# Performance work log

Hardware: AMD Instinct MI355X
Metric: run time of the kernel (lower is better)

The kernel has to match this reference:

```python
import jax, jax.numpy as jnp
import numpy as np

H, D, DM, L, B = 16, 64, 1024, 256, 64
SCALE = 1.0 / np.sqrt(D)   # 1/sqrt(d_head)
CHUNK = 64
LN_EPS = 1e-5


def setup_inputs() -> dict:
    key = jax.random.key(0)
    k0, k1, k2, k3 = jax.random.split(key, 4)
    h = jax.random.normal(k0, (L, B, DM), jnp.float32)
    qkv_w = jax.random.normal(k1, (H * 4 * D, DM), jnp.float32) * 0.02
    o_w = jax.random.normal(k2, (DM, H * D), jnp.float32) * 0.02
    ln_gamma = jnp.ones((DM,), jnp.float32)
    ln_beta = jnp.zeros((DM,), jnp.float32)
    pi0 = jax.random.uniform(k3, (H, 256), jnp.float32)
    return {"h": h, "qkv_w": qkv_w, "o_w": o_w,
            "ln_gamma": ln_gamma, "ln_beta": ln_beta, "pi0": pi0}


def _phi(x):
    # elu(x) + 1, then sum-normalize over feature dim
    e = jax.nn.elu(x) + 1.0
    return e / e.sum(-1, keepdims=True)


def _fast_weight_sum(q, k, v):
    # q,k,v: [B,H,L,D]. out[t] = q_t @ W_t, W_t = sum_{s<=t} k_s v_s^T (inclusive).
    # Chunked-recurrent form: intra-chunk causal GEMM + inter-chunk carried state.
    Bb, Hh, Ll, Dd = q.shape
    nc = Ll // CHUNK
    rs = lambda x: x.reshape(Bb, Hh, nc, CHUNK, Dd).transpose(2, 0, 1, 3, 4)  # [nc,B,H,C,D]
    qc, kc, vc = rs(q), rs(k), rs(v)
    mask = jnp.tril(jnp.ones((CHUNK, CHUNK), q.dtype))  # inclusive causal

    def step(W, xs):
        qi, ki, vi = xs  # [B,H,C,D]
        scores = jnp.einsum('bhtd,bhsd->bhts', qi, ki) * mask
        out = jnp.einsum('bhts,bhsd->bhtd', scores, vi) \
            + jnp.einsum('bhtd,bhde->bhte', qi, W)
        W = W + jnp.einsum('bhsd,bhse->bhde', ki, vi)
        return W, out

    W0 = jnp.zeros((Bb, Hh, Dd, Dd), q.dtype)
    _, outs = jax.lax.scan(step, W0, (qc, kc, vc))  # outs: [nc,B,H,C,D]
    return outs.transpose(1, 2, 0, 3, 4).reshape(Bb, Hh, Ll, Dd)


def reference(h, qkv_w, o_w, ln_gamma, ln_beta, pi0):
    slen, bsz, _ = h.shape
    # qkv projection and head split (rbf2keys: q, k1, k2, v)
    qkv = (h @ qkv_w.T).reshape(slen, bsz, H, 4 * D)
    hq, hk1, hk2, hv = jnp.split(qkv, 4, axis=-1)       # each [L,B,H,D]
    perm = lambda x: x.transpose(1, 2, 0, 3)            # -> [B,H,L,D]
    hq, hk1, hk2, hv = perm(hq), perm(hk1), perm(hk2), perm(hv)

    hq = _phi(hq)
    hk1 = _phi(hk1)
    hk2 = _phi(hk2)

    out1 = _fast_weight_sum(hq, hk1, hv)
    out2 = _fast_weight_sum(hq, hk2, hv)

    # skip_attn_normalization=True path: pi0-gated mixture of the two memories
    p = jnp.clip(pi0, 0.0, 1.0)[None, :, :slen, None]   # [1,H,L,1]
    layer_out = SCALE * (out1 * p + out2 * (1.0 - p))   # [B,H,L,D]

    # [B,H,L,D] -> [L,B,H*D]
    layer_out = layer_out.transpose(0, 2, 1, 3).reshape(bsz, slen, H * D).transpose(1, 0, 2)
    attn_out = layer_out @ o_w.T                        # [L,B,DM]

    # post-LN residual (pre_lnorm=False)
    x = h + attn_out
    mu = x.mean(-1, keepdims=True)
    var = ((x - mu) ** 2).mean(-1, keepdims=True)
    return (x - mu) / jnp.sqrt(var + LN_EPS) * ln_gamma + ln_beta
```

## Files before the change

kernel.cpp:

```cpp
#include <hip/hip_runtime.h>
#include <type_traits>


typedef short v8s __attribute__((ext_vector_type(8)));
typedef float v4f __attribute__((ext_vector_type(4)));

__device__ __forceinline__ float bf2f(short s) {
    unsigned int u = ((unsigned int)(unsigned short)s) << 16;
    float f;
    __builtin_memcpy(&f, &u, 4);
    return f;
}
__device__ __forceinline__ short f2bf(float f) {
    unsigned int u;
    __builtin_memcpy(&u, &f, 4);
    u = u + 0x7fffu + ((u >> 16) & 1u);
    return (short)(u >> 16);
}

__device__ __forceinline__ void load_lds16(const short* g, short* l) {
    __builtin_amdgcn_global_load_lds((const __attribute__((address_space(1))) void*)g,
                                     (__attribute__((address_space(3))) void*)l, 16, 0, 0);
}

__global__ void __launch_bounds__(256)
cvt_bf16(const float* __restrict__ in, short* __restrict__ out, int n4) {
    int i = blockIdx.x * 256 + threadIdx.x;
    if (i >= n4) return;
    float4 v = ((const float4*)in)[i];
    short4 o;
    o.x = f2bf(v.x); o.y = f2bf(v.y); o.z = f2bf(v.z); o.w = f2bf(v.w);
    ((short4*)out)[i] = o;
}

template <typename OutT>
__global__ void __launch_bounds__(256)
gemm_nt(const short* __restrict__ A, const short* __restrict__ B,
        OutT* __restrict__ C, int M, int N, int K) {
    constexpr int BM = 128, BK = 32;
    __shared__ __align__(16) short sA[BM * BK];
    __shared__ __align__(16) short sB[BM * BK];
    const int tid = threadIdx.x;
    const int bm = blockIdx.x, bn = blockIdx.y;
    const int lane = tid & 63, w = tid >> 6;
    const int wy = w >> 1, wx = w & 1;
    const int lr = lane & 15, lq = lane >> 4;

    v4f acc[4][4] = {};

    const int srow = 32 * w + (lane >> 2);
    const int scol = (lane & 3) * 8;
    const short* gA0 = A + (long)(bm * BM + srow) * K + scol;
    const short* gB0 = B + (long)(bn * BM + srow) * K + scol;
    short* lA0 = sA + 32 * w * BK;
    short* lB0 = sB + 32 * w * BK;

    for (int kt = 0; kt < K; kt += BK) {
        __syncthreads();
        load_lds16(gA0 + kt, lA0);
        load_lds16(gA0 + 16 * K + kt, lA0 + 16 * BK);
        load_lds16(gB0 + kt, lB0);
        load_lds16(gB0 + 16 * K + kt, lB0 + 16 * BK);
        __syncthreads();

        v8s af[4], bfv[4];
#pragma unroll
        for (int i = 0; i < 4; i++)
            af[i] = *(const v8s*)&sA[(wy * 64 + i * 16 + lr) * BK + lq * 8];
#pragma unroll
        for (int j = 0; j < 4; j++)
            bfv[j] = *(const v8s*)&sB[(wx * 64 + j * 16 + lr) * BK + lq * 8];
#pragma unroll
        for (int i = 0; i < 4; i++)
#pragma unroll
            for (int j = 0; j < 4; j++)
                acc[i][j] = __builtin_amdgcn_mfma_f32_16x16x32_bf16(af[i], bfv[j], acc[i][j], 0, 0, 0);
    }
#pragma unroll
    for (int i = 0; i < 4; i++)
#pragma unroll
        for (int j = 0; j < 4; j++)
#pragma unroll
            for (int r = 0; r < 4; r++) {
                int row = bm * BM + wy * 64 + i * 16 + lq * 4 + r;
                int col = bn * BM + wx * 64 + j * 16 + lr;
                float v = acc[i][j][r];
                if constexpr (std::is_same_v<OutT, short>)
                    C[(long)row * N + col] = f2bf(v);
                else
                    C[(long)row * N + col] = v;
            }
}

#define SW(row, s) ((row) * 72 + ((((s) >> 3) ^ (((row) >> 4) & 7)) << 3) + ((s) & 7))

__global__ void __launch_bounds__(256)
fastweight(const short* __restrict__ qkv, short* __restrict__ out1, short* __restrict__ out2) {
    const int bid = blockIdx.x;
    const int mem = bid & 1, h = (bid >> 1) & 15, b = bid >> 5;
    const int tid = threadIdx.x;
    const int w = tid >> 6, lane = tid & 63;
    const int lq = lane >> 4, lr = lane & 15;
    __shared__ __align__(16) short sq[64 * 72];
    __shared__ __align__(16) short skS[64 * 72];
    __shared__ __align__(16) short skT[64 * 72];
    __shared__ __align__(16) short svT[64 * 72];
    __shared__ __align__(16) short sWT[64 * 72];
    short* outbuf = mem ? out2 : out1;
    const int koff = 64 + mem * 64;

    for (int i = tid; i < 64 * 36; i += 256) ((int*)sWT)[i] = 0;

    const int r = tid >> 2, seg = (tid & 3) * 16;

    v4f wacc[4] = {};

    for (int c = 0; c < 4; c++) {
        __syncthreads();
        const long gbase = ((long)((c * 64 + r) * 64 + b)) * 4096 + h * 256;
        {
            union { int4 v[2]; short s[16]; } u;
            u.v[0] = *(const int4*)(qkv + gbase + seg);
            u.v[1] = *(const int4*)(qkv + gbase + seg + 8);
            float f[16]; float ssum = 0.f;
#pragma unroll
            for (int i = 0; i < 16; i++) {
                float x = bf2f(u.s[i]);
                float e = x > 0.f ? x + 1.f : __expf(x);
                f[i] = e; ssum += e;
            }
            ssum += __shfl_xor(ssum, 1, 64);
            ssum += __shfl_xor(ssum, 2, 64);
            float inv = 1.f / ssum;
            union { int4 v[2]; short s[16]; } o;
#pragma unroll
            for (int i = 0; i < 16; i++) o.s[i] = f2bf(f[i] * inv);
            *(int4*)&sq[SW(r, seg)] = o.v[0];
            *(int4*)&sq[SW(r, seg + 8)] = o.v[1];
        }
        {
            union { int4 v[2]; short s[16]; } u;
            u.v[0] = *(const int4*)(qkv + gbase + koff + seg);
            u.v[1] = *(const int4*)(qkv + gbase + koff + seg + 8);
            float f[16]; float ssum = 0.f;
#pragma unroll
            for (int i = 0; i < 16; i++) {
                float x = bf2f(u.s[i]);
                float e = x > 0.f ? x + 1.f : __expf(x);
                f[i] = e; ssum += e;
            }
            ssum += __shfl_xor(ssum, 1, 64);
            ssum += __shfl_xor(ssum, 2, 64);
            float inv = 1.f / ssum;
            union { int4 v[2]; short s[16]; } o;
#pragma unroll
            for (int i = 0; i < 16; i++) o.s[i] = f2bf(f[i] * inv);
            *(int4*)&skS[SW(r, seg)] = o.v[0];
            *(int4*)&skS[SW(r, seg + 8)] = o.v[1];
#pragma unroll
            for (int i = 0; i < 16; i++) skT[SW(seg + i, r)] = o.s[i];
        }
        {
            union { int4 v[2]; short s[16]; } u;
            u.v[0] = *(const int4*)(qkv + gbase + 192 + seg);
            u.v[1] = *(const int4*)(qkv + gbase + 192 + seg + 8);
#pragma unroll
            for (int i = 0; i < 16; i++) svT[SW(seg + i, r)] = u.s[i];
        }
        __syncthreads();

        v8s qa0 = *(const v8s*)&sq[SW(16 * w + lr, lq * 8)];
        v8s qa1 = *(const v8s*)&sq[SW(16 * w + lr, 32 + lq * 8)];

        v4f sacc[4];
#pragma unroll
        for (int n = 0; n < 4; n++) {
            v8s b0 = *(const v8s*)&skS[SW(16 * n + lr, lq * 8)];
            v8s b1 = *(const v8s*)&skS[SW(16 * n + lr, 32 + lq * 8)];
            v4f t = {};
            t = __builtin_amdgcn_mfma_f32_16x16x32_bf16(qa0, b0, t, 0, 0, 0);
            t = __builtin_amdgcn_mfma_f32_16x16x32_bf16(qa1, b1, t, 0, 0, 0);
            sacc[n] = t;
        }
        __syncthreads();
#pragma unroll
        for (int n = 0; n < 4; n++)
#pragma unroll
            for (int rr = 0; rr < 4; rr++) {
                int t_ = 16 * w + lq * 4 + rr;
                int s_ = 16 * n + lr;
                skS[SW(t_, s_)] = f2bf(s_ <= t_ ? sacc[n][rr] : 0.f);
            }

        v8s sa0 = *(const v8s*)&skS[SW(16 * w + lr, lq * 8)];
        v8s sa1 = *(const v8s*)&skS[SW(16 * w + lr, 32 + lq * 8)];
        v4f oacc[4];
#pragma unroll
        for (int n = 0; n < 4; n++) {
            v8s vb0 = *(const v8s*)&svT[SW(16 * n + lr, lq * 8)];
            v8s vb1 = *(const v8s*)&svT[SW(16 * n + lr, 32 + lq * 8)];
            v8s wb0 = *(const v8s*)&sWT[SW(16 * n + lr, lq * 8)];
            v8s wb1 = *(const v8s*)&sWT[SW(16 * n + lr, 32 + lq * 8)];
            v4f t = {};
            t = __builtin_amdgcn_mfma_f32_16x16x32_bf16(sa0, vb0, t, 0, 0, 0);
            t = __builtin_amdgcn_mfma_f32_16x16x32_bf16(sa1, vb1, t, 0, 0, 0);
            t = __builtin_amdgcn_mfma_f32_16x16x32_bf16(qa0, wb0, t, 0, 0, 0);
            t = __builtin_amdgcn_mfma_f32_16x16x32_bf16(qa1, wb1, t, 0, 0, 0);
            oacc[n] = t;
        }
#pragma unroll
        for (int n = 0; n < 4; n++)
#pragma unroll
            for (int rr = 0; rr < 4; rr++) {
                int t_ = 16 * w + lq * 4 + rr;
                long o = ((long)((c * 64 + t_) * 64 + b)) * 1024 + h * 64 + 16 * n + lr;
                outbuf[o] = f2bf(oacc[n][rr]);
            }

        if (c < 3) {
            __syncthreads();
            v8s va0 = *(const v8s*)&svT[SW(16 * w + lr, lq * 8)];
            v8s va1 = *(const v8s*)&svT[SW(16 * w + lr, 32 + lq * 8)];
#pragma unroll
            for (int n = 0; n < 4; n++) {
                v8s kb0 = *(const v8s*)&skT[SW(16 * n + lr, lq * 8)];
                v8s kb1 = *(const v8s*)&skT[SW(16 * n + lr, 32 + lq * 8)];
                wacc[n] = __builtin_amdgcn_mfma_f32_16x16x32_bf16(va0, kb0, wacc[n], 0, 0, 0);
                wacc[n] = __builtin_amdgcn_mfma_f32_16x16x32_bf16(va1, kb1, wacc[n], 0, 0, 0);
            }
#pragma unroll
            for (int n = 0; n < 4; n++)
#pragma unroll
                for (int rr = 0; rr < 4; rr++)
                    sWT[SW(16 * w + lq * 4 + rr, 16 * n + lr)] = f2bf(wacc[n][rr]);
        }
    }
}

__global__ void __launch_bounds__(256)
mix_kernel(const short* __restrict__ l1, const short* __restrict__ l2,
           const float* __restrict__ pi0, short* __restrict__ outm) {
    long idx8 = ((long)blockIdx.x * 256 + threadIdx.x) * 8;
    int col = (int)(idx8 & 1023);
    int row = (int)(idx8 >> 10);
    int hh = col >> 6;
    int l = row >> 6;
    float p = pi0[hh * 256 + l];
    p = fminf(fmaxf(p, 0.f), 1.f);
    float q = 1.f - p;
    union { int4 v; short s[8]; } ua, ub, uo;
    ua.v = *(const int4*)(l1 + idx8);
    ub.v = *(const int4*)(l2 + idx8);
#pragma unroll
    for (int i = 0; i < 8; i++)
        uo.s[i] = f2bf(0.125f * (p * bf2f(ua.s[i]) + q * bf2f(ub.s[i])));
    *(int4*)(outm + idx8) = uo.v;
}

__global__ void __launch_bounds__(256)
ln_kernel(const float* __restrict__ h, const float* __restrict__ attn,
          const float* __restrict__ gamma, const float* __restrict__ beta,
          float* __restrict__ out) {
    const int row = blockIdx.x;
    const long base = (long)row * 1024;
    const int tid = threadIdx.x;
    float4 xh = ((const float4*)(h + base))[tid];
    float4 xa = ((const float4*)(attn + base))[tid];
    float4 x;
    x.x = xh.x + xa.x; x.y = xh.y + xa.y; x.z = xh.z + xa.z; x.w = xh.w + xa.w;
    float s = x.x + x.y + x.z + x.w;
    float s2 = x.x * x.x + x.y * x.y + x.z * x.z + x.w * x.w;
#pragma unroll
    for (int m = 32; m > 0; m >>= 1) {
        s += __shfl_xor(s, m, 64);
        s2 += __shfl_xor(s2, m, 64);
    }
    __shared__ float ps[4], ps2[4];
    int w = tid >> 6, lane = tid & 63;
    if (lane == 0) { ps[w] = s; ps2[w] = s2; }
    __syncthreads();
    s = ps[0] + ps[1] + ps[2] + ps[3];
    s2 = ps2[0] + ps2[1] + ps2[2] + ps2[3];
    float mu = s * (1.f / 1024.f);
    float var = s2 * (1.f / 1024.f) - mu * mu;
    float inv = rsqrtf(var + 1e-5f);
    float4 g = ((const float4*)gamma)[tid];
    float4 bb = ((const float4*)beta)[tid];
    float4 o;
    o.x = (x.x - mu) * inv * g.x + bb.x;
    o.y = (x.y - mu) * inv * g.y + bb.y;
    o.z = (x.z - mu) * inv * g.z + bb.z;
    o.w = (x.w - mu) * inv * g.w + bb.w;
    ((float4*)(out + base))[tid] = o;
}

extern "C" void kernel_launch(void* const* d_in, const int* in_sizes, int n_in,
                              void* d_out, int out_size, void* d_ws, size_t ws_size,
                              hipStream_t stream) {
    const float* h     = (const float*)d_in[0];
    const float* qkvw  = (const float*)d_in[1];
    const float* ow    = (const float*)d_in[2];
    const float* gamma = (const float*)d_in[3];
    const float* beta  = (const float*)d_in[4];
    const float* pi0   = (const float*)d_in[5];
    float* out = (float*)d_out;
    char* ws = (char*)d_ws;

    short* h_bf   = (short*)(ws);
    short* wq_bf  = (short*)(ws + 33554432);
    short* wo_bf  = (short*)(ws + 41943040);
    short* qkv_bf = (short*)(ws + 44040192);
    short* l1     = (short*)(ws + 178257920);
    short* l2     = (short*)(ws + 211812352);
    float* attnf  = (float*)(ws + 44040192);
    short* lmix   = h_bf;

    cvt_bf16<<<16384, 256, 0, stream>>>(h, h_bf, 16777216 / 4);
    cvt_bf16<<<4096, 256, 0, stream>>>(qkvw, wq_bf, 4194304 / 4);
    cvt_bf16<<<1024, 256, 0, stream>>>(ow, wo_bf, 1048576 / 4);

    gemm_nt<short><<<dim3(128, 32), 256, 0, stream>>>(h_bf, wq_bf, qkv_bf, 16384, 4096, 1024);

    fastweight<<<2048, 256, 0, stream>>>(qkv_bf, l1, l2);

    mix_kernel<<<8192, 256, 0, stream>>>(l1, l2, pi0, lmix);

    gemm_nt<float><<<dim3(128, 8), 256, 0, stream>>>(lmix, wo_bf, attnf, 16384, 1024, 1024);

    ln_kernel<<<16384, 256, 0, stream>>>(h, attnf, gamma, beta, out);
}
```

Baseline: 463.1 us.

## Rewrite bf16 GEMM as 256x256 double-buffered pipelined kernel with swizzled LDS

Replaces the simple 128x128 tile GEMM, which synchronises twice per K step, with a 256x256 tile, 512-thread kernel. It double-buffers LDS with a 64-wide K tile, interleaves global-to-LDS staging with MFMA quarters under explicit barriers and vmcnt waits, XOR-swizzles LDS to avoid bank conflicts, and remaps block IDs for L2 locality. The aim is to hide load latency and raise MFMA utilisation in both projection GEMMs. The cost is heavy register pressure from 32 accumulator tiles and 128 KB of LDS, which permits only one block per CU, plus fragile hand-tuned synchronisation.

```diff
diff --git a/kernel.cpp b/kernel.cpp
--- a/kernel.cpp
+++ b/kernel.cpp
@@ -34,57 +34,126 @@
 }
 
 template <typename OutT>
-__global__ void __launch_bounds__(256)
-gemm_nt(const short* __restrict__ A, const short* __restrict__ B,
+__global__ void __launch_bounds__(512, 2)
+gemm_nt(const short* __restrict__ Ap, const short* __restrict__ Bp,
         OutT* __restrict__ C, int M, int N, int K) {
-    constexpr int BM = 128, BK = 32;
-    __shared__ __align__(16) short sA[BM * BK];
-    __shared__ __align__(16) short sB[BM * BK];
+    __shared__ __align__(16) short lds[2][2][256 * 64];
+
     const int tid = threadIdx.x;
-    const int bm = blockIdx.x, bn = blockIdx.y;
-    const int lane = tid & 63, w = tid >> 6;
-    const int wy = w >> 1, wx = w & 1;
-    const int lr = lane & 15, lq = lane >> 4;
-
-    v4f acc[4][4] = {};
-
-    const int srow = 32 * w + (lane >> 2);
-    const int scol = (lane & 3) * 8;
-    const short* gA0 = A + (long)(bm * BM + srow) * K + scol;
-    const short* gB0 = B + (long)(bn * BM + srow) * K + scol;
-    short* lA0 = sA + 32 * w * BK;
-    short* lB0 = sB + 32 * w * BK;
-
-    for (int kt = 0; kt < K; kt += BK) {
-        __syncthreads();
-        load_lds16(gA0 + kt, lA0);
-        load_lds16(gA0 + 16 * K + kt, lA0 + 16 * BK);
-        load_lds16(gB0 + kt, lB0);
-        load_lds16(gB0 + 16 * K + kt, lB0 + 16 * BK);
-        __syncthreads();
-
-        v8s af[4], bfv[4];
-#pragma unroll
-        for (int i = 0; i < 4; i++)
-            af[i] = *(const v8s*)&sA[(wy * 64 + i * 16 + lr) * BK + lq * 8];
-#pragma unroll
-        for (int j = 0; j < 4; j++)
-            bfv[j] = *(const v8s*)&sB[(wx * 64 + j * 16 + lr) * BK + lq * 8];
-#pragma unroll
-        for (int i = 0; i < 4; i++)
-#pragma unroll
-            for (int j = 0; j < 4; j++)
-                acc[i][j] = __builtin_amdgcn_mfma_f32_16x16x32_bf16(af[i], bfv[j], acc[i][j], 0, 0, 0);
+    const int w = tid >> 6, lane = tid & 63;
+    const int wm = w >> 2, wn = w & 3;
+    const int lq = lane >> 4, lr = lane & 15;
+    const int asw = (lr & 7) * 8;
+    const int rr = tid >> 3;
+    const int scol = ((tid & 7) * 8) ^ ((rr & 7) * 8);
+
+    int bid = blockIdx.y * gridDim.x + blockIdx.x;
+    int nwg = gridDim.x * gridDim.y;
+    int swz = (bid & 7) * (nwg >> 3) + (bid >> 3);
+    int bm = swz % gridDim.x, bn = swz / gridDim.x;
+
+    v4f acc[8][4] = {};
+    v8s a[4][2];
+    v8s b[2][2][2];
+
+    const int NT = K >> 6;
+    const int nIter = NT >> 1;
+
+#define BAR_() do { asm volatile("" ::: "memory"); __builtin_amdgcn_s_barrier(); asm volatile("" ::: "memory"); } while (0)
+#define VMCNT4_() asm volatile("s_waitcnt vmcnt(4)" ::: "memory")
+#define STAGE_(MAT, BUF, HALF, KT) do { \
+        const short* g_ = ((MAT) ? Bp : Ap) + \
+            (long)(((MAT) ? bn : bm) * 256 + (HALF) * 128 + rr) * K + (KT) * 64 + scol; \
+        short* l_ = &lds[BUF][MAT][(HALF) * 8192] + w * 512; \
+        load_lds16(g_, l_); \
+        load_lds16(g_ + (long)64 * K, l_ + 4096); \
+    } while (0)
+#define LDA_(QM, BUF) do { \
+        _Pragma("unroll") \
+        for (int mi = 0; mi < 4; ++mi) { \
+            const short* pa_ = &lds[BUF][0][(wm * 128 + (QM) * 64 + mi * 16 + lr) * 64]; \
+            a[mi][0] = *(const v8s*)&pa_[(lq * 8) ^ asw]; \
+            a[mi][1] = *(const v8s*)&pa_[(32 + lq * 8) ^ asw]; \
+        } \
+    } while (0)
+#define LDB_(QN, BUF) do { \
+        _Pragma("unroll") \
+        for (int ni = 0; ni < 2; ++ni) { \
+            const short* pb_ = &lds[BUF][1][(wn * 64 + (QN) * 32 + ni * 16 + lr) * 64]; \
+            b[QN][ni][0] = *(const v8s*)&pb_[(lq * 8) ^ asw]; \
+            b[QN][ni][1] = *(const v8s*)&pb_[(32 + lq * 8) ^ asw]; \
+        } \
+    } while (0)
+#define MFMA_(QM, QN) do { \
+        __builtin_amdgcn_s_setprio(1); \
+        _Pragma("unroll") \
+        for (int kk = 0; kk < 2; ++kk) \
+            _Pragma("unroll") \
+            for (int mi = 0; mi < 4; ++mi) \
+                _Pragma("unroll") \
+                for (int ni = 0; ni < 2; ++ni) \
+                    acc[(QM) * 4 + mi][(QN) * 2 + ni] = __builtin_amdgcn_mfma_f32_16x16x32_bf16( \
+                        a[mi][kk], b[QN][ni][kk], acc[(QM) * 4 + mi][(QN) * 2 + ni], 0, 0, 0); \
+        __builtin_amdgcn_s_setprio(0); \
+    } while (0)
+
+    STAGE_(1, 0, 0, 0);
+    STAGE_(1, 0, 1, 0);
+    STAGE_(0, 0, 0, 0);
+    STAGE_(0, 0, 1, 0);
+    STAGE_(1, 1, 0, 1);
+    STAGE_(1, 1, 1, 1);
+    VMCNT4_();
+    BAR_();
+
+    for (int it = 0; it < nIter; ++it) {
+        const int t = 2 * it;
+        const int t1 = t + 1;
+        int t2 = t + 2; if (t2 >= NT) t2 -= NT;
+        int t3 = t + 3; if (t3 >= NT) t3 -= NT;
+
+        LDA_(0, 0); LDB_(0, 0);
+        STAGE_(0, 1, 0, t1);
+        BAR_(); MFMA_(0, 0); BAR_();
+        LDB_(1, 0);
+        STAGE_(0, 1, 1, t1);
+        BAR_(); MFMA_(0, 1); BAR_();
+        LDA_(1, 0);
+        STAGE_(1, 0, 0, t2);
+        BAR_(); MFMA_(1, 0); BAR_();
+        STAGE_(1, 0, 1, t2);
+        VMCNT4_();
+        BAR_(); MFMA_(1, 1); BAR_();
+        LDA_(0, 1); LDB_(0, 1);
+        STAGE_(0, 0, 0, t2);
+        BAR_(); MFMA_(0, 0); BAR_();
+        LDB_(1, 1);
+        STAGE_(0, 0, 1, t2);
+        BAR_(); MFMA_(0, 1); BAR_();
+        LDA_(1, 1);
+        STAGE_(1, 1, 0, t3);
+        BAR_(); MFMA_(1, 0); BAR_();
+        STAGE_(1, 1, 1, t3);
+        VMCNT4_();
+        BAR_(); MFMA_(1, 1); BAR_();
     }
-#pragma unroll
-    for (int i = 0; i < 4; i++)
-#pragma unroll
-        for (int j = 0; j < 4; j++)
-#pragma unroll
-            for (int r = 0; r < 4; r++) {
-                int row = bm * BM + wy * 64 + i * 16 + lq * 4 + r;
-                int col = bn * BM + wx * 64 + j * 16 + lr;
-                float v = acc[i][j][r];
+
+#undef BAR_
+#undef VMCNT4_
+#undef STAGE_
+#undef LDA_
+#undef LDB_
+#undef MFMA_
+
+#pragma unroll
+    for (int m = 0; m < 8; ++m)
+#pragma unroll
+        for (int n = 0; n < 4; ++n)
+#pragma unroll
+            for (int r = 0; r < 4; ++r) {
+                int row = bm * 256 + wm * 128 + m * 16 + lq * 4 + r;
+                int col = bn * 256 + wn * 64 + n * 16 + lr;
+                float v = acc[m][n][r];
                 if constexpr (std::is_same_v<OutT, short>)
                     C[(long)row * N + col] = f2bf(v);
                 else
@@ -319,13 +388,13 @@
     cvt_bf16<<<4096, 256, 0, stream>>>(qkvw, wq_bf, 4194304 / 4);
     cvt_bf16<<<1024, 256, 0, stream>>>(ow, wo_bf, 1048576 / 4);
 
-    gemm_nt<short><<<dim3(128, 32), 256, 0, stream>>>(h_bf, wq_bf, qkv_bf, 16384, 4096, 1024);
+    gemm_nt<short><<<dim3(64, 16), 512, 0, stream>>>(h_bf, wq_bf, qkv_bf, 16384, 4096, 1024);
 
     fastweight<<<2048, 256, 0, stream>>>(qkv_bf, l1, l2);
 
     mix_kernel<<<8192, 256, 0, stream>>>(l1, l2, pi0, lmix);
 
-    gemm_nt<float><<<dim3(128, 8), 256, 0, stream>>>(lmix, wo_bf, attnf, 16384, 1024, 1024);
+    gemm_nt<float><<<dim3(64, 4), 512, 0, stream>>>(lmix, wo_bf, attnf, 16384, 1024, 1024);
 
     ln_kernel<<<16384, 256, 0, stream>>>(h, attnf, gamma, beta, out);
 }
```

After: 415.9 us. -10.2%, faster.
